# Kernel optimization log

Measured on AMD Instinct MI355X. Metric: run time of the kernel, lower is better.

Reference implementation:

```python
import jax, jax.numpy as jnp
import numpy as np

D_MODEL, N_HEADS, D_FF = 512, 8, 2048
D_K = D_MODEL // N_HEADS
EPS = 1e-5


def layer_norm(x, g, b):
    mu = jnp.mean(x, axis=-1, keepdims=True)
    var = jnp.mean(jnp.square(x - mu), axis=-1, keepdims=True)
    return (x - mu) * jax.lax.rsqrt(var + EPS) * g + b


def setup_inputs() -> dict:
    key = jax.random.key(0)
    ks = jax.random.split(key, 12)
    B, S = 2, 2048
    s_attn = 1.0 / np.sqrt(D_MODEL)
    s_ff1 = 1.0 / np.sqrt(D_MODEL)
    s_ff2 = 1.0 / np.sqrt(D_FF)
    inp = {
        "x": jax.random.normal(ks[0], (B, S, D_MODEL), dtype=jnp.float32),
        "mask": jnp.ones((B, 1, 1, S), dtype=jnp.int32),
        "Wq": jax.random.normal(ks[1], (D_MODEL, D_MODEL), jnp.float32) * s_attn,
        "bq": jnp.zeros((D_MODEL,), jnp.float32),
        "Wk": jax.random.normal(ks[2], (D_MODEL, D_MODEL), jnp.float32) * s_attn,
        "bk": jnp.zeros((D_MODEL,), jnp.float32),
        "Wv": jax.random.normal(ks[3], (D_MODEL, D_MODEL), jnp.float32) * s_attn,
        "bv": jnp.zeros((D_MODEL,), jnp.float32),
        "Wo": jax.random.normal(ks[4], (D_MODEL, D_MODEL), jnp.float32) * s_attn,
        "bo": jnp.zeros((D_MODEL,), jnp.float32),
        "W1": jax.random.normal(ks[5], (D_MODEL, D_FF), jnp.float32) * s_ff1,
        "b1": jnp.zeros((D_FF,), jnp.float32),
        "W2": jax.random.normal(ks[6], (D_FF, D_MODEL), jnp.float32) * s_ff2,
        "b2": jnpp.zeros((D_MODEL,), jnp.float32) if False else jnp.zeros((D_MODEL,), jnp.float32),
        "g1": jnp.ones((D_MODEL,), jnp.float32),
        "beta1": jnp.zeros((D_MODEL,), jnp.float32),
        "g2": jnp.ones((D_MODEL,), jnp.float32),
        "beta2": jnp.zeros((D_MODEL,), jnp.float32),
    }
    return inp


def reference(x, mask, Wq, bq, Wk, bk, Wv, bv, Wo, bo, W1, b1, W2, b2, g1, beta1, g2, beta2):
    B, S, _ = x.shape
    # projections -> [B, H, S, Dk]
    def split_heads(t):
        return t.reshape(B, S, N_HEADS, D_K).transpose(0, 2, 1, 3)
    q = split_heads(x @ Wq + bq)
    k = split_heads(x @ Wk + bk)
    v = split_heads(x @ Wv + bv)
    scores = jnp.einsum("bhqd,bhkd->bhqk", q, k) / np.sqrt(D_K)
    scores = jnp.where(mask == 0, jnp.float32(-1e9), scores)
    attn = jax.nn.softmax(scores, axis=-1)
    ctx = jnp.einsum("bhqk,bhkd->bhqd", attn, v)
    ctx = ctx.transpose(0, 2, 1, 3).reshape(B, S, D_MODEL)
    attn_out = ctx @ Wo + bo
    x1 = layer_norm(x + attn_out, g1, beta1)
    ff = jax.nn.relu(x1 @ W1 + b1) @ W2 + b2
    return layer_norm(x1 + ff, g2, beta2)
```

## Files before the change

### kernel.cpp

```cpp
#include <hip/hip_runtime.h>
#include <hip/hip_bf16.h>


#define D_MODEL 512
#define N_HEADS 8
#define D_K 64
#define D_FF 2048
#define BATCH 2
#define SEQ 2048
#define NROWS (BATCH * SEQ)

typedef __hip_bfloat16 bf16;
typedef __attribute__((ext_vector_type(8))) short bf16x8;
typedef __attribute__((ext_vector_type(4))) float f32x4;

__device__ __forceinline__ unsigned short f2b(float f) {
  union { bf16 b; unsigned short u; } cv;
  cv.b = __float2bfloat16(f);
  return cv.u;
}
__device__ __forceinline__ float b2f(unsigned short u) {
  return __uint_as_float(((unsigned int)u) << 16);
}
__device__ __forceinline__ float toF(const bf16 x) { return __bfloat162float(x); }
__device__ __forceinline__ float toF(const float x) { return x; }
__device__ __forceinline__ void storeC(float* p, float v) { *p = v; }
__device__ __forceinline__ void storeC(bf16* p, float v) {
  *p = __float2bfloat16(v);
}

__device__ __forceinline__ void ld8f(const float* p, float* v) {
  const float4 a = *(const float4*)p;
  const float4 b = *(const float4*)(p + 4);
  v[0] = a.x; v[1] = a.y; v[2] = a.z; v[3] = a.w;
  v[4] = b.x; v[5] = b.y; v[6] = b.z; v[7] = b.w;
}
__device__ __forceinline__ void ld8f(const bf16* p, float* v) {
  const bf16x8 u = *(const bf16x8*)p;
#pragma unroll
  for (int i = 0; i < 8; ++i) v[i] = b2f((unsigned short)u[i]);
}
__device__ __forceinline__ void st8f(float* p, const float* v) {
  *(float4*)p = make_float4(v[0], v[1], v[2], v[3]);
  *(float4*)(p + 4) = make_float4(v[4], v[5], v[6], v[7]);
}
__device__ __forceinline__ void st8f(bf16* p, const float* v) {
  bf16x8 u;
#pragma unroll
  for (int i = 0; i < 8; ++i) u[i] = (short)f2b(v[i]);
  *(bf16x8*)p = u;
}

#define WT_Q 0
#define WT_K 262144
#define WT_V 524288
#define WT_O 786432
#define WT_1 1048576
#define WT_2 2097152

__global__ __launch_bounds__(256) void prep_kernel(
    const float* __restrict__ Wq, const float* __restrict__ Wk,
    const float* __restrict__ Wv, const float* __restrict__ Wo,
    const float* __restrict__ W1, const float* __restrict__ W2,
    bf16* __restrict__ outw, const float* __restrict__ x,
    bf16* __restrict__ xb) {
  const int z = blockIdx.z;
  const int t = threadIdx.x;

  if (z == 6) {
    const size_t base =
        ((size_t)(blockIdx.y * 32 + blockIdx.x) * 2048) + (size_t)t * 8;
    float v[8];
    ld8f(x + base, v);
    st8f(xb + base, v);
    return;
  }

  const float* W;
  int R, Cn;
  size_t off;
  if (z == 0)      { W = Wq; R = 512;  Cn = 512;  off = WT_Q; }
  else if (z == 1) { W = Wk; R = 512;  Cn = 512;  off = WT_K; }
  else if (z == 2) { W = Wv; R = 512;  Cn = 512;  off = WT_V; }
  else if (z == 3) { W = Wo; R = 512;  Cn = 512;  off = WT_O; }
  else if (z == 4) { W = W1; R = 512;  Cn = 2048; off = WT_1; }
  else             { W = W2; R = 2048; Cn = 512;  off = WT_2; }
  const int c0 = blockIdx.x * 64;
  const int r0 = blockIdx.y * 64;
  if (c0 >= Cn || r0 >= R) return;

  __shared__ short tile[64][72];
  {
    const int r = t >> 2, cg = (t & 3) * 16;
    const float* src = &W[(size_t)(r0 + r) * Cn + c0 + cg];
#pragma unroll
    for (int i = 0; i < 4; ++i) {
      const float4 v = *(const float4*)(src + 4 * i);
      tile[cg + 4 * i + 0][r] = (short)f2b(v.x);
      tile[cg + 4 * i + 1][r] = (short)f2b(v.y);
      tile[cg + 4 * i + 2][r] = (short)f2b(v.z);
      tile[cg + 4 * i + 3][r] = (short)f2b(v.w);
    }
  }
  __syncthreads();
  {
    const int c = t >> 2, rg = (t & 3) * 16;
    short* dst = (short*)outw + off + (size_t)(c0 + c) * R + r0 + rg;
    *(bf16x8*)dst = *(const bf16x8*)&tile[c][rg];
    *(bf16x8*)(dst + 8) = *(const bf16x8*)&tile[c][rg + 8];
  }
}

template <int BM, bool RELU, bool RESID>
__global__ __launch_bounds__(256) void gemm_bf16_kernel(
    const bf16* __restrict__ A, int lda,
    const bf16* __restrict__ Wt0, const bf16* __restrict__ Wt1,
    const bf16* __restrict__ Wt2, int ldk,
    const float* __restrict__ b0, const float* __restrict__ b1,
    const float* __restrict__ b2,
    bf16* __restrict__ C0, bf16* __restrict__ C1, bf16* __restrict__ C2,
    int ldc, int K, const bf16* __restrict__ R) {
  const bf16* Wt = (blockIdx.z == 0) ? Wt0 : (blockIdx.z == 1 ? Wt1 : Wt2);
  const float* bias = (blockIdx.z == 0) ? b0 : (blockIdx.z == 1 ? b1 : b2);
  bf16* C = (blockIdx.z == 0) ? C0 : (blockIdx.z == 1 ? C1 : C2);

  constexpr int RG = BM / 64;
  constexpr int NA = BM / 32;

  __shared__ short as_[BM][72];
  __shared__ short bs[64][72];

  const int rowBase = blockIdx.y * BM;
  const int colBase = blockIdx.x * 64;
  const int t = threadIdx.x;
  const int wave = t >> 6;
  const int lane = t & 63;
  const int quad = lane >> 4;
  const int l15 = lane & 15;

  const int arow = (BM == 64) ? (t >> 2) : (t >> 1);
  const int akc = (BM == 64) ? ((t & 3) * 16) : ((t & 1) * 32);
  const int srow = t >> 2;
  const int skc = (t & 3) * 16;

  const short* Abase = (const short*)A + (size_t)(rowBase + arow) * lda + akc;
  const short* Wbase = (const short*)Wt + (size_t)(colBase + srow) * ldk + skc;

  bf16x8 areg[NA], wreg[2];
#pragma unroll
  for (int i = 0; i < NA; ++i) areg[i] = *(const bf16x8*)(Abase + 8 * i);
  wreg[0] = *(const bf16x8*)(Wbase);
  wreg[1] = *(const bf16x8*)(Wbase + 8);

  f32x4 acc[RG][4];
#pragma unroll
  for (int i = 0; i < RG; ++i)
#pragma unroll
    for (int nt = 0; nt < 4; ++nt) acc[i][nt] = (f32x4){0.f, 0.f, 0.f, 0.f};

  for (int k0 = 0; k0 < K; k0 += 64) {
#pragma unroll
    for (int i = 0; i < NA; ++i) *(bf16x8*)&as_[arow][akc + 8 * i] = areg[i];
    *(bf16x8*)&bs[srow][skc] = wreg[0];
    *(bf16x8*)&bs[srow][skc + 8] = wreg[1];

    if (k0 + 64 < K) {
      const short* ap = Abase + k0 + 64;
      const short* wp = Wbase + k0 + 64;
#pragma unroll
      for (int i = 0; i < NA; ++i) areg[i] = *(const bf16x8*)(ap + 8 * i);
      wreg[0] = *(const bf16x8*)(wp);
      wreg[1] = *(const bf16x8*)(wp + 8);
    }
    __syncthreads();

#pragma unroll
    for (int kc = 0; kc < 2; ++kc) {
      bf16x8 af[RG];
#pragma unroll
      for (int i = 0; i < RG; ++i)
        af[i] = *(const bf16x8*)
            &as_[wave * (16 * RG) + i * 16 + l15][quad * 8 + kc * 32];
#pragma unroll
      for (int nt = 0; nt < 4; ++nt) {
        const bf16x8 bfr =
            *(const bf16x8*)&bs[nt * 16 + l15][quad * 8 + kc * 32];
#pragma unroll
        for (int i = 0; i < RG; ++i)
          acc[i][nt] = __builtin_amdgcn_mfma_f32_16x16x32_bf16(
              af[i], bfr, acc[i][nt], 0, 0, 0);
      }
    }
    __syncthreads();
  }

#pragma unroll
  for (int i = 0; i < RG; ++i)
#pragma unroll
    for (int nt = 0; nt < 4; ++nt) {
      const int col = colBase + nt * 16 + l15;
#pragma unroll
      for (int r = 0; r < 4; ++r) {
        const int row = rowBase + wave * (16 * RG) + i * 16 + quad * 4 + r;
        float v = acc[i][nt][r] + bias[col];
        if (RESID) v += toF(R[(size_t)row * ldc + col]);
        if (RELU) v = fmaxf(v, 0.f);
        storeC(&C[(size_t)row * ldc + col], v);
      }
    }
}

__global__ __launch_bounds__(512) void attn_mfma_kernel(
    const bf16* __restrict__ Q, const bf16* __restrict__ Km,
    const bf16* __restrict__ V, const int* __restrict__ mask,
    bf16* __restrict__ ctx) {
  const int qt = blockIdx.x;
  const int bh = blockIdx.y;
  const int b = bh >> 3;
  const int h = bh & 7;
  const int t = threadIdx.x;
  const int wave = t >> 6;
  const int half = wave >> 2;
  const int wq = wave & 3;
  const int lane = t & 63;
  const int quad = lane >> 4;
  const int l15 = lane & 15;

  __shared__ __align__(16) char smem[74240];
  auto ks = (short(*)[64][72])(smem);
  auto vt = (short(*)[64][72])(smem + 18432);
  auto pb = (short(*)[32][72])(smem + 36864);
  auto mk = (int(*)[64])(smem + 73728);
  auto mg = (float(*)[32][68])(smem);

  bf16x8 qf[2][2];
#pragma unroll
  for (int rg = 0; rg < 2; ++rg) {
    const short* qg = (const short*)Q +
        (size_t)(b * SEQ + qt * 128 + wq * 32 + rg * 16 + l15) * D_MODEL +
        h * D_K + quad * 8;
    qf[rg][0] = *(const bf16x8*)qg;
    qf[rg][1] = *(const bf16x8*)(qg + 32);
  }

  f32x4 of[2][4];
#pragma unroll
  for (int rg = 0; rg < 2; ++rg)
#pragma unroll
    for (int nt = 0; nt < 4; ++nt) of[rg][nt] = (f32x4){0.f, 0.f, 0.f, 0.f};
  float l_acc[2][4] = {{0.f, 0.f, 0.f, 0.f}, {0.f, 0.f, 0.f, 0.f}};

  const int hs = t >> 8;
  const int tt = t & 255;
  const int kr = tt >> 2, kc0 = (tt & 3) * 16;
  const int vk = tt & 63, vc0 = ((tt >> 6) & 3) * 16;

  bf16x8 kv0, kv1, vv0, vv1;
  int mv = 1;
  {
    const int keyRow = (hs * 16 + 0) * 64;
    const short* kg = (const short*)Km +
        (size_t)(b * SEQ + keyRow + kr) * D_MODEL + h * D_K + kc0;
    kv0 = *(const bf16x8*)kg;
    kv1 = *(const bf16x8*)(kg + 8);
    const short* vg = (const short*)V +
        (size_t)(b * SEQ + keyRow + vk) * D_MODEL + h * D_K + vc0;
    vv0 = *(const bf16x8*)vg;
    vv1 = *(const bf16x8*)(vg + 8);
    if (tt < 64) mv = mask[b * SEQ + keyRow + tt];
  }

  for (int kt = 0; kt < 16; ++kt) {
    *(bf16x8*)&ks[hs][kr][kc0] = kv0;
    *(bf16x8*)&ks[hs][kr][kc0 + 8] = kv1;
#pragma unroll
    for (int i = 0; i < 8; ++i) vt[hs][vc0 + i][vk] = vv0[i];
#pragma unroll
    for (int i = 0; i < 8; ++i) vt[hs][vc0 + 8 + i][vk] = vv1[i];
    if (tt < 64) mk[hs][tt] = mv;

    if (kt + 1 < 16) {
      const int keyRow = (hs * 16 + kt + 1) * 64;
      const short* kg = (const short*)Km +
          (size_t)(b * SEQ + keyRow + kr) * D_MODEL + h * D_K + kc0;
      kv0 = *(const bf16x8*)kg;
      kv1 = *(const bf16x8*)(kg + 8);
      const short* vg = (const short*)V +
          (size_t)(b * SEQ + keyRow + vk) * D_MODEL + h * D_K + vc0;
      vv0 = *(const bf16x8*)vg;
      vv1 = *(const bf16x8*)(vg + 8);
      if (tt < 64) mv = mask[b * SEQ + keyRow + tt];
    }
    __syncthreads();

    f32x4 sf[2][4];
#pragma unroll
    for (int nt = 0; nt < 4; ++nt) {
      const bf16x8 kf0 = *(const bf16x8*)&ks[half][l15 + 16 * nt][quad * 8];
      const bf16x8 kf1 =
          *(const bf16x8*)&ks[half][l15 + 16 * nt][quad * 8 + 32];
#pragma unroll
      for (int rg = 0; rg < 2; ++rg) {
        f32x4 acc = (f32x4){0.f, 0.f, 0.f, 0.f};
        acc = __builtin_amdgcn_mfma_f32_16x16x32_bf16(qf[rg][0], kf0, acc, 0, 0, 0);
        acc = __builtin_amdgcn_mfma_f32_16x16x32_bf16(qf[rg][1], kf1, acc, 0, 0, 0);
        sf[rg][nt] = acc;
      }
    }

#pragma unroll
    for (int nt = 0; nt < 4; ++nt) {
      const bool dead = (mk[half][l15 + 16 * nt] == 0);
#pragma unroll
      for (int rg = 0; rg < 2; ++rg)
#pragma unroll
        for (int r = 0; r < 4; ++r) {
          float p = __expf(fmaf(sf[rg][nt][r], 0.125f, -8.f));
          if (dead) p = 0.f;
          l_acc[rg][r] += p;
          pb[wave][rg * 16 + quad * 4 + r][l15 + 16 * nt] = (short)f2b(p);
        }
    }

#pragma unroll
    for (int kc = 0; kc < 2; ++kc) {
      bf16x8 pf[2];
#pragma unroll
      for (int rg = 0; rg < 2; ++rg)
        pf[rg] = *(const bf16x8*)&pb[wave][rg * 16 + l15][kc * 32 + quad * 8];
#pragma unroll
      for (int nt = 0; nt < 4; ++nt) {
        const bf16x8 vf =
            *(const bf16x8*)&vt[half][l15 + 16 * nt][kc * 32 + quad * 8];
#pragma unroll
        for (int rg = 0; rg < 2; ++rg)
          of[rg][nt] = __builtin_amdgcn_mfma_f32_16x16x32_bf16(
              pf[rg], vf, of[rg][nt], 0, 0, 0);
      }
    }
    __syncthreads();
  }

#pragma unroll
  for (int xm = 1; xm < 16; xm <<= 1)
#pragma unroll
    for (int rg = 0; rg < 2; ++rg)
#pragma unroll
      for (int r = 0; r < 4; ++r)
        l_acc[rg][r] += __shfl_xor(l_acc[rg][r], xm, 64);

#pragma unroll
  for (int rg = 0; rg < 2; ++rg)
#pragma unroll
    for (int nt = 0; nt < 4; ++nt)
#pragma unroll
      for (int r = 0; r < 4; ++r)
        mg[wave][rg * 16 + quad * 4 + r][l15 + 16 * nt] = of[rg][nt][r];
  if (l15 == 0) {
#pragma unroll
    for (int rg = 0; rg < 2; ++rg)
#pragma unroll
      for (int r = 0; r < 4; ++r)
        mg[wave][rg * 16 + quad * 4 + r][64] = l_acc[rg][r];
  }
  __syncthreads();

  if (wave < 4) {
    const int pw = wave + 4;
#pragma unroll
    for (int rg = 0; rg < 2; ++rg)
#pragma unroll
      for (int r = 0; r < 4; ++r) {
        const int qrow = rg * 16 + quad * 4 + r;
        const float inv = 1.f / (l_acc[rg][r] + mg[pw][qrow][64]);
        const int row = qt * 128 + wave * 32 + qrow;
        bf16* cp = ctx + (size_t)(b * SEQ + row) * D_MODEL + h * D_K;
#pragma unroll
        for (int nt = 0; nt < 4; ++nt)
          cp[l15 + 16 * nt] = __float2bfloat16(
              (of[rg][nt][r] + mg[pw][qrow][l15 + 16 * nt]) * inv);
      }
  }
}

template <typename BT, typename OT>
__global__ __launch_bounds__(256) void ln_kernel(
    const BT* __restrict__ base, const float* __restrict__ g,
    const float* __restrict__ beta, OT* __restrict__ out) {
  const int wave = threadIdx.x >> 6;
  const int lane = threadIdx.x & 63;
  const int row = blockIdx.x * 4 + wave;
  const size_t rb = (size_t)row * D_MODEL + lane * 8;

  float v[8];
  ld8f(base + rb, v);

  float s = 0.f;
#pragma unroll
  for (int i = 0; i < 8; ++i) s += v[i];
#pragma unroll
  for (int xm = 1; xm < 64; xm <<= 1) s += __shfl_xor(s, xm, 64);
  const float mu = s * (1.f / (float)D_MODEL);

  float q = 0.f;
#pragma unroll
  for (int i = 0; i < 8; ++i) {
    v[i] -= mu;
    q += v[i] * v[i];
  }
#pragma unroll
  for (int xm = 1; xm < 64; xm <<= 1) q += __shfl_xor(q, xm, 64);
  const float rs = rsqrtf(q * (1.f / (float)D_MODEL) + 1e-5f);

  float gv[8], bv[8];
  ld8f(g + lane * 8, gv);
  ld8f(beta + lane * 8, bv);
#pragma unroll
  for (int i = 0; i < 8; ++i) v[i] = v[i] * rs * gv[i] + bv[i];
  st8f(out + rb, v);
}

extern "C" void kernel_launch(void* const* d_in, const int* in_sizes, int n_in,
                              void* d_out, int out_size, void* d_ws, size_t ws_size,
                              hipStream_t stream) {
  const float* x     = (const float*)d_in[0];
  const int*   mask  = (const int*)d_in[1];
  const float* Wq    = (const float*)d_in[2];
  const float* bq    = (const float*)d_in[3];
  const float* Wk    = (const float*)d_in[4];
  const float* bk    = (const float*)d_in[5];
  const float* Wv    = (const float*)d_in[6];
  const float* bv    = (const float*)d_in[7];
  const float* Wo    = (const float*)d_in[8];
  const float* bo    = (const float*)d_in[9];
  const float* W1    = (const float*)d_in[10];
  const float* b1    = (const float*)d_in[11];
  const float* W2    = (const float*)d_in[12];
  const float* b2    = (const float*)d_in[13];
  const float* g1    = (const float*)d_in[14];
  const float* beta1 = (const float*)d_in[15];
  const float* g2    = (const float*)d_in[16];
  const float* beta2 = (const float*)d_in[17];
  float* out = (float*)d_out;

  char* ws = (char*)d_ws;
  const size_t MB4 = (size_t)NROWS * D_MODEL * sizeof(bf16);
  bf16* q        = (bf16*)(ws + 0 * MB4);
  bf16* kbuf     = (bf16*)(ws + 1 * MB4);
  bf16* vbuf     = (bf16*)(ws + 2 * MB4);
  bf16* ctx      = (bf16*)(ws + 3 * MB4);
  bf16* xb       = (bf16*)(ws + 4 * MB4);
  bf16* attn_out = q;
  bf16* x1       = kbuf;
  bf16* ffacc    = vbuf;
  bf16* ffmid    = (bf16*)(ws + 4 * MB4);

  bf16* wt = (bf16*)d_out;

  const dim3 blk(256);

  prep_kernel<<<dim3(32, 32, 7), blk, 0, stream>>>(Wq, Wk, Wv, Wo, W1, W2, wt,
                                                   x, xb);

  gemm_bf16_kernel<128, false, false>
      <<<dim3(D_MODEL / 64, NROWS / 128, 3), blk, 0, stream>>>(
          xb, D_MODEL, wt + WT_Q, wt + WT_K, wt + WT_V, D_MODEL,
          bq, bk, bv, q, kbuf, vbuf, D_MODEL, D_MODEL, nullptr);

  attn_mfma_kernel<<<dim3(SEQ / 128, BATCH * N_HEADS), dim3(512), 0, stream>>>(
      q, kbuf, vbuf, mask, ctx);

  gemm_bf16_kernel<64, false, true>
      <<<dim3(D_MODEL / 64, NROWS / 64, 1), blk, 0, stream>>>(
          ctx, D_MODEL, wt + WT_O, wt + WT_O, wt + WT_O, D_MODEL,
          bo, bo, bo, attn_out, attn_out, attn_out, D_MODEL, D_MODEL, xb);

  ln_kernel<bf16, bf16><<<NROWS / 4, blk, 0, stream>>>(attn_out, g1, beta1, x1);

  gemm_bf16_kernel<128, true, false>
      <<<dim3(D_FF / 64, NROWS / 128, 1), blk, 0, stream>>>(
          x1, D_MODEL, wt + WT_1, wt + WT_1, wt + WT_1, D_MODEL,
          b1, b1, b1, ffmid, ffmid, ffmid, D_FF, D_MODEL, nullptr);

  gemm_bf16_kernel<64, false, true>
      <<<dim3(D_MODEL / 64, NROWS / 64, 1), blk, 0, stream>>>(
          ffmid, D_FF, wt + WT_2, wt + WT_2, wt + WT_2, D_FF,
          b2, b2, b2, ffacc, ffacc, ffacc, D_MODEL, D_FF, x1);

  ln_kernel<bf16, float><<<NROWS / 4, blk, 0, stream>>>(ffacc, g2, beta2, out);
}
```

Measured before the change: 208.3 us.

## Load GEMM tiles directly into LDS via global_load_lds in chunk-major layout

The bf16 GEMM kernel no longer stages A and W tiles through registers before writing them to shared memory. It now issues global_load_lds 16-byte copies straight into LDS. The shared layout changes from padded row-major to a chunk-major [k-chunk][row][8] arrangement, and the MFMA fragment reads are re-indexed to match. This removes the ds_write instructions and staging registers, but also drops the register-based prefetch of the next K tile, so global loads no longer overlap with compute. Correctness also depends on the barrier waiting for the async LDS writes to finish.

Measured after the change: 245.3 us. 1.18x slower.

```diff
diff --git a/kernel.cpp b/kernel.cpp
--- a/kernel.cpp
+++ b/kernel.cpp
@@ -27,6 +27,12 @@
 __device__ __forceinline__ void storeC(float* p, float v) { *p = v; }
 __device__ __forceinline__ void storeC(bf16* p, float v) {
   *p = __float2bfloat16(v);
+}
+
+__device__ __forceinline__ void dma16(const void* g, void* l) {
+  __builtin_amdgcn_global_load_lds(
+      (const __attribute__((address_space(1))) unsigned int*)g,
+      (__attribute__((address_space(3))) unsigned int*)l, 16, 0, 0);
 }
 
 __device__ __forceinline__ void ld8f(const float* p, float* v) {
@@ -125,10 +131,11 @@
   bf16* C = (blockIdx.z == 0) ? C0 : (blockIdx.z == 1 ? C1 : C2);
 
   constexpr int RG = BM / 64;
-  constexpr int NA = BM / 32;
-
-  __shared__ short as_[BM][72];
-  __shared__ short bs[64][72];
+  constexpr int AI = BM / 32;
+  constexpr int RSH = (BM == 64) ? 6 : 7;
+
+  __shared__ __align__(16) short asA[8 * BM * 8];
+  __shared__ __align__(16) short bsW[8 * 64 * 8];
 
   const int rowBase = blockIdx.y * BM;
   const int colBase = blockIdx.x * 64;
@@ -138,20 +145,6 @@
   const int quad = lane >> 4;
   const int l15 = lane & 15;
 
-  const int arow = (BM == 64) ? (t >> 2) : (t >> 1);
-  const int akc = (BM == 64) ? ((t & 3) * 16) : ((t & 1) * 32);
-  const int srow = t >> 2;
-  const int skc = (t & 3) * 16;
-
-  const short* Abase = (const short*)A + (size_t)(rowBase + arow) * lda + akc;
-  const short* Wbase = (const short*)Wt + (size_t)(colBase + srow) * ldk + skc;
-
-  bf16x8 areg[NA], wreg[2];
-#pragma unroll
-  for (int i = 0; i < NA; ++i) areg[i] = *(const bf16x8*)(Abase + 8 * i);
-  wreg[0] = *(const bf16x8*)(Wbase);
-  wreg[1] = *(const bf16x8*)(Wbase + 8);
-
   f32x4 acc[RG][4];
 #pragma unroll
   for (int i = 0; i < RG; ++i)
@@ -160,17 +153,20 @@
 
   for (int k0 = 0; k0 < K; k0 += 64) {
 #pragma unroll
-    for (int i = 0; i < NA; ++i) *(bf16x8*)&as_[arow][akc + 8 * i] = areg[i];
-    *(bf16x8*)&bs[srow][skc] = wreg[0];
-    *(bf16x8*)&bs[srow][skc + 8] = wreg[1];
-
-    if (k0 + 64 < K) {
-      const short* ap = Abase + k0 + 64;
-      const short* wp = Wbase + k0 + 64;
-#pragma unroll
-      for (int i = 0; i < NA; ++i) areg[i] = *(const bf16x8*)(ap + 8 * i);
-      wreg[0] = *(const bf16x8*)(wp);
-      wreg[1] = *(const bf16x8*)(wp + 8);
+    for (int i = 0; i < AI; ++i) {
+      const int s = (wave * AI + i) * 64 + lane;
+      const int c = s >> RSH;
+      const int row = s & (BM - 1);
+      dma16((const short*)A + (size_t)(rowBase + row) * lda + k0 + c * 8,
+            (char*)asA + (size_t)(wave * AI + i) * 1024);
+    }
+#pragma unroll
+    for (int i = 0; i < 2; ++i) {
+      const int s = (wave * 2 + i) * 64 + lane;
+      const int c = s >> 6;
+      const int row = s & 63;
+      dma16((const short*)Wt + (size_t)(colBase + row) * ldk + k0 + c * 8,
+            (char*)bsW + (size_t)(wave * 2 + i) * 1024);
     }
     __syncthreads();
 
@@ -180,11 +176,11 @@
 #pragma unroll
       for (int i = 0; i < RG; ++i)
         af[i] = *(const bf16x8*)
-            &as_[wave * (16 * RG) + i * 16 + l15][quad * 8 + kc * 32];
+            &asA[((quad + 4 * kc) * BM + wave * (16 * RG) + i * 16 + l15) * 8];
 #pragma unroll
       for (int nt = 0; nt < 4; ++nt) {
         const bf16x8 bfr =
-            *(const bf16x8*)&bs[nt * 16 + l15][quad * 8 + kc * 32];
+            *(const bf16x8*)&bsW[((quad + 4 * kc) * 64 + nt * 16 + l15) * 8];
 #pragma unroll
         for (int i = 0; i < RG; ++i)
           acc[i][nt] = __builtin_amdgcn_mfma_f32_16x16x32_bf16(
```
